# Kernel optimization log

Measured on AMD Instinct MI355X. Metric: run time of the kernel, lower is better.

Reference implementation:

```python
import jax, jax.numpy as jnp
import numpy as np

B, T, D, H = 512, 1024, 64, 64     # batch, time, input_size, hidden_size
R = 4                              # number of reward heads
MH = 32                            # MLP hidden size


def setup_inputs() -> dict:
    key = jax.random.key(0)
    ks = jax.random.split(key, 16)
    s = lambda k, shape, scale=1.0: jax.random.normal(k, shape, dtype=jnp.float32) * scale
    inp = {
        "x": s(ks[0], (B, T, D)),
        # learned initial states (nn.Parameter randn(1,1,H) -> store as (H,))
        "h_init": s(ks[1], (H,)),
        "c_init": s(ks[2], (H,)),
        # LSTM params, PyTorch layout: W_ih (4H, D), W_hh (4H, H), gate order i,f,g,o
        "W_ih": s(ks[3], (4 * H, D), 1.0 / np.sqrt(H)),
        "W_hh": s(ks[4], (4 * H, H), 1.0 / np.sqrt(H)),
        "b_ih": s(ks[5], (4 * H,), 1.0 / np.sqrt(H)),
        "b_hh": s(ks[6], (4 * H,), 1.0 / np.sqrt(H)),
        # R stacked MLP heads: Linear(H,MH) -> ReLU -> Linear(MH,MH) -> ReLU -> Linear(MH,1)
        "W1": s(ks[7], (R, MH, H), 1.0 / np.sqrt(H)),
        "b1": s(ks[8], (R, MH), 1.0 / np.sqrt(H)),
        "W2": s(ks[9], (R, MH, MH), 1.0 / np.sqrt(MH)),
        "b2": s(ks[10], (R, MH), 1.0 / np.sqrt(MH)),
        "W3": s(ks[11], (R, 1, MH), 1.0 / np.sqrt(MH)),
        "b3": s(ks[12], (R, 1), 1.0 / np.sqrt(MH)),
    }
    return inp


def _lstm(x, h0, c0, W_ih, W_hh, b_ih, b_hh):
    # x: (B, T, D). Returns y: (B, T, H).
    Hh = h0.shape[-1]
    b = b_ih + b_hh                      # (4H,)
    # precompute input projections for all steps: (T, B, 4H)
    xg = jnp.einsum('btd,gd->tbg', x, W_ih) + b

    def step(carry, xg_t):
        h, c = carry                     # (B, H) each
        gates = xg_t + h @ W_hh.T        # (B, 4H)
        i, f, g, o = jnp.split(gates, 4, axis=-1)
        c = jax.nn.sigmoid(f) * c + jax.nn.sigmoid(i) * jnp.tanh(g)
        h = jax.nn.sigmoid(o) * jnp.tanh(c)
        return (h, c), h

    Bb = x.shape[0]
    h0b = jnp.broadcast_to(h0, (Bb, Hh))
    c0b = jnp.broadcast_to(c0, (Bb, Hh))
    _, ys = jax.lax.scan(step, (h0b, c0b), xg)   # ys: (T, B, H)
    return jnp.transpose(ys, (1, 0, 2))


def _heads(y, W1, b1, W2, b2, W3, b3):
    # y: (B, T, H) -> (R, B, T); all R heads computed in one batched einsum chain
    h1 = jax.nn.relu(jnp.einsum('bth,rmh->rbtm', y, W1) + b1[:, None, None, :])
    h2 = jax.nn.relu(jnp.einsum('rbtm,rnm->rbtn', h1, W2) + b2[:, None, None, :])
    out = jnp.einsum('rbtn,ron->rbto', h2, W3) + b3[:, None, None, :]
    return out[..., 0]                   # squeeze last dim -> (R, B, T)


def reference(x, h_init, c_init, W_ih, W_hh, b_ih, b_hh, W1, b1, W2, b2, W3, b3):
    y = _lstm(x, h_init, c_init, W_ih, W_hh, b_ih, b_hh)
    outs = _heads(y, W1, b1, W2, b2, W3, b3)   # (R, B, T); row r == rewards[r] head
    return (y, outs)
```

## Files before the change

### kernel.cpp

```cpp
#include <hip/hip_runtime.h>

#define BB 512
#define TT 1024
#define DD 64
#define HH 64
#define BT (BB * TT)
#define Y_SIZE (BB * TT * HH)

typedef _Float16 half8 __attribute__((ext_vector_type(8)));
typedef _Float16 half4 __attribute__((ext_vector_type(4)));
typedef float f32x4 __attribute__((ext_vector_type(4)));

#define MFMA16(a, b, c) __builtin_amdgcn_mfma_f32_16x16x32_f16((a), (b), (c), 0, 0, 0)

__device__ __forceinline__ void wg_barrier_lds() {
    asm volatile("s_waitcnt lgkmcnt(0)" ::: "memory");
    __builtin_amdgcn_s_barrier();
    asm volatile("" ::: "memory");
}

__device__ __forceinline__ float sigm(float x) {
    return __builtin_amdgcn_rcpf(1.0f + __expf(-x));
}
__device__ __forceinline__ float tanh_(float x) {
    return 1.0f - 2.0f * __builtin_amdgcn_rcpf(1.0f + __expf(2.0f * x));
}

__device__ __forceinline__ half8 cvt8(f32x4 a, f32x4 b) {
    half8 h;
    h[0] = (_Float16)a[0]; h[1] = (_Float16)a[1];
    h[2] = (_Float16)a[2]; h[3] = (_Float16)a[3];
    h[4] = (_Float16)b[0]; h[5] = (_Float16)b[1];
    h[6] = (_Float16)b[2]; h[7] = (_Float16)b[3];
    return h;
}

__global__ __launch_bounds__(256) void lstm_kernel(
    const float* __restrict__ x, const float* __restrict__ h_init,
    const float* __restrict__ c_init, const float* __restrict__ W_ih,
    const float* __restrict__ W_hh, const float* __restrict__ b_ih,
    const float* __restrict__ b_hh, float* __restrict__ y)
{
    __shared__ alignas(16) _Float16 xch[2][16][2][72];
    __shared__ alignas(16) _Float16 hst[2][2][HH];
    __shared__ float xg[16][2][265];

    const int tid  = threadIdx.x;
    const int wave = tid >> 6;
    const int lane = tid & 63;
    const int col  = lane & 15;
    const int quad = lane >> 4;
    const int sel  = (lane >> 3) & 1;
    const int r_act = lane >> 5;
    const int j    = (wave << 4) + col;
    const bool writer = ((lane >> 4) & 1) == 0;

    const int b0 = blockIdx.x * 2;

    half8 bf[4][4];
    f32x4 biasv[4];
#pragma unroll
    for (int G = 0; G < 4; ++G) {
        const int n = (G << 6) + j;
        const float bs = b_ih[n] + b_hh[n];
        biasv[G][0] = bs; biasv[G][1] = bs; biasv[G][2] = bs; biasv[G][3] = bs;
#pragma unroll
        for (int c = 0; c < 4; ++c) {
            const float* src = (c < 2) ? (W_ih + n * DD + c * 32 + quad * 8)
                                       : (W_hh + n * HH + (c - 2) * 32 + quad * 8);
            f32x4 w0 = *(const f32x4*)src;
            f32x4 w1 = *(const f32x4*)(src + 4);
            bf[G][c] = cvt8(w0, w1);
        }
    }

    float c_state = c_init[j];

    if (tid < 128) {
        const int rr = tid >> 6, jj = tid & 63;
        hst[0][rr][jj] = (_Float16)h_init[jj];
    }
    {
        const int ss = tid >> 4, rr = (tid >> 3) & 1, j0 = (tid & 7) << 3;
        const float* src = x + ((b0 + rr) * TT + ss) * DD + j0;
        f32x4 g0 = *(const f32x4*)src;
        f32x4 g1 = *(const f32x4*)(src + 4);
        *(half8*)&xch[0][ss][rr][j0] = cvt8(g0, g1);
    }
    wg_barrier_lds();

    const int ss_pf = tid >> 4, rr_pf = (tid >> 3) & 1, j0_pf = (tid & 7) << 3;

    for (int ci = 0; ci < 64; ++ci) {
        const int buf = ci & 1;
        const bool pf = (ci + 1) < 64;
        f32x4 g0, g1;
        if (pf) {
            const float* src = x + ((b0 + rr_pf) * TT + ((ci + 1) << 4) + ss_pf) * DD + j0_pf;
            g0 = *(const f32x4*)src;
            g1 = *(const f32x4*)(src + 4);
        }

#pragma unroll
        for (int rr = 0; rr < 2; ++rr) {
            half8 ax0 = *(const half8*)&xch[buf][col][rr][quad * 8];
            half8 ax1 = *(const half8*)&xch[buf][col][rr][32 + quad * 8];
#pragma unroll
            for (int G = 0; G < 4; ++G) {
                f32x4 d = MFMA16(ax0, bf[G][0], biasv[G]);
                d = MFMA16(ax1, bf[G][1], d);
#pragma unroll
                for (int r = 0; r < 4; ++r)
                    xg[(quad << 2) + r][rr][(G << 6) + j] = d[r];
            }
        }

#pragma unroll
        for (int s = 0; s < 16; ++s) {
            const int t = (ci << 4) + s;
            const int p = s & 1;

            const float xg0 = xg[s][r_act][0 * 64 + j];
            const float xg1 = xg[s][r_act][1 * 64 + j];
            const float xg2 = xg[s][r_act][2 * 64 + j];
            const float xg3 = xg[s][r_act][3 * 64 + j];
            const _Float16* hrow = &hst[p][sel][0];
            half8 a2 = *(const half8*)(hrow + quad * 8);
            half8 a3 = *(const half8*)(hrow + 32 + quad * 8);

            f32x4 c0 = {xg0, xg0, xg0, xg0};
            f32x4 c1 = {xg1, xg1, xg1, xg1};
            f32x4 c2 = {xg2, xg2, xg2, xg2};
            f32x4 c3 = {xg3, xg3, xg3, xg3};
            f32x4 acc0 = MFMA16(a2, bf[0][2], c0);
            f32x4 acc1 = MFMA16(a2, bf[1][2], c1);
            f32x4 acc2 = MFMA16(a2, bf[2][2], c2);
            f32x4 acc3 = MFMA16(a2, bf[3][2], c3);
            acc0 = MFMA16(a3, bf[0][3], acc0); acc1 = MFMA16(a3, bf[1][3], acc1);
            acc2 = MFMA16(a3, bf[2][3], acc2); acc3 = MFMA16(a3, bf[3][3], acc3);

            const float si = sigm(acc0[0]);
            const float sf = sigm(acc1[0]);
            const float tg = tanh_(acc2[0]);
            const float so = sigm(acc3[0]);
            c_state = sf * c_state + si * tg;
            const float hv = so * tanh_(c_state);
            if (writer) {
                hst[p ^ 1][r_act][j] = (_Float16)hv;
                y[((b0 + r_act) * TT + t) * HH + j] = hv;
            }
            if (s == 14 && pf) {
                *(half8*)&xch[buf ^ 1][ss_pf][rr_pf][j0_pf] = cvt8(g0, g1);
            }
            wg_barrier_lds();
        }
    }
}

__global__ __launch_bounds__(256) void heads_kernel(
    const float* __restrict__ y,
    const float* __restrict__ W1, const float* __restrict__ b1,
    const float* __restrict__ W2, const float* __restrict__ b2,
    const float* __restrict__ W3, const float* __restrict__ b3,
    float* __restrict__ outs)
{
    __shared__ alignas(16) _Float16 h1w[4][2][16][144];
    __shared__ alignas(16) _Float16 h2w[4][2][16][144];

    const int tid  = threadIdx.x;
    const int wave = tid >> 6;
    const int lane = tid & 63;
    const int col  = lane & 15;
    const int quad = lane >> 4;

    half8 w1f[8][2]; float bias1[8];
#pragma unroll
    for (int nt = 0; nt < 8; ++nt) {
        const int n = nt * 16 + col;
        bias1[nt] = b1[n];
#pragma unroll
        for (int c = 0; c < 2; ++c) {
            const float* src = W1 + n * 64 + c * 32 + quad * 8;
            w1f[nt][c] = cvt8(*(const f32x4*)src, *(const f32x4*)(src + 4));
        }
    }
    half8 w2f[8]; float bias2[8];
#pragma unroll
    for (int nt = 0; nt < 8; ++nt) {
        const int n = nt * 16 + col;
        bias2[nt] = b2[n];
        const float* src = W2 + n * 32 + quad * 8;
        w2f[nt] = cvt8(*(const f32x4*)src, *(const f32x4*)(src + 4));
    }
    half8 b3f[4];
    {
        const float* src = W3 + (col < 4 ? col * 32 : 0) + quad * 8;
        half8 wv = cvt8(*(const f32x4*)src, *(const f32x4*)(src + 4));
        half8 hz;
#pragma unroll
        for (int i = 0; i < 8; ++i) hz[i] = (_Float16)0.0f;
#pragma unroll
        for (int kc = 0; kc < 4; ++kc)
            b3f[kc] = (col == kc) ? wv : hz;
    }
    const float b3v = (col < 4) ? b3[col] : 0.0f;

    const long wbase = (long)blockIdx.x * 256 + wave * 64;

    f32x4 ga0, ga1, ga2, ga3;
    {
        const float* src = y + (wbase + col) * 64 + quad * 8;
        ga0 = *(const f32x4*)src;       ga1 = *(const f32x4*)(src + 4);
        ga2 = *(const f32x4*)(src + 32); ga3 = *(const f32x4*)(src + 36);
    }

#pragma unroll
    for (int tb = 0; tb < 4; ++tb) {
        const int pb = tb & 1;
        half8 a0 = cvt8(ga0, ga1);
        half8 a1 = cvt8(ga2, ga3);
        if (tb < 3) {
            const float* src = y + (wbase + (tb + 1) * 16 + col) * 64 + quad * 8;
            ga0 = *(const f32x4*)src;       ga1 = *(const f32x4*)(src + 4);
            ga2 = *(const f32x4*)(src + 32); ga3 = *(const f32x4*)(src + 36);
        }

#pragma unroll
        for (int nt = 0; nt < 8; ++nt) {
            f32x4 acc = {bias1[nt], bias1[nt], bias1[nt], bias1[nt]};
            acc = MFMA16(a0, w1f[nt][0], acc);
            acc = MFMA16(a1, w1f[nt][1], acc);
#pragma unroll
            for (int r = 0; r < 4; ++r) {
                float v = acc[r] > 0.0f ? acc[r] : 0.0f;
                h1w[wave][pb][(quad << 2) + r][nt * 16 + col] = (_Float16)v;
            }
        }
        half8 ah[4];
#pragma unroll
        for (int hd = 0; hd < 4; ++hd)
            ah[hd] = *(const half8*)&h1w[wave][pb][col][hd * 32 + quad * 8];
#pragma unroll
        for (int nt = 0; nt < 8; ++nt) {
            f32x4 acc = {bias2[nt], bias2[nt], bias2[nt], bias2[nt]};
            acc = MFMA16(ah[nt >> 1], w2f[nt], acc);
#pragma unroll
            for (int r = 0; r < 4; ++r) {
                float v = acc[r] > 0.0f ? acc[r] : 0.0f;
                h2w[wave][pb][(quad << 2) + r][nt * 16 + col] = (_Float16)v;
            }
        }
        f32x4 d = {b3v, b3v, b3v, b3v};
#pragma unroll
        for (int kc = 0; kc < 4; ++kc) {
            half8 av = *(const half8*)&h2w[wave][pb][col][kc * 32 + quad * 8];
            d = MFMA16(av, b3f[kc], d);
        }
        if (col < 4)
            *(f32x4*)(outs + (long)col * BT + wbase + tb * 16 + quad * 4) = d;
    }
}

extern "C" void kernel_launch(void* const* d_in, const int* in_sizes, int n_in,
                              void* d_out, int out_size, void* d_ws, size_t ws_size,
                              hipStream_t stream) {
    (void)in_sizes; (void)n_in; (void)out_size; (void)d_ws; (void)ws_size;
    const float* x      = (const float*)d_in[0];
    const float* h_init = (const float*)d_in[1];
    const float* c_init = (const float*)d_in[2];
    const float* W_ih   = (const float*)d_in[3];
    const float* W_hh   = (const float*)d_in[4];
    const float* b_ih   = (const float*)d_in[5];
    const float* b_hh   = (const float*)d_in[6];
    const float* W1     = (const float*)d_in[7];
    const float* b1     = (const float*)d_in[8];
    const float* W2     = (const float*)d_in[9];
    const float* b2     = (const float*)d_in[10];
    const float* W3     = (const float*)d_in[11];
    const float* b3     = (const float*)d_in[12];
    float* y    = (float*)d_out;
    float* outs = y + Y_SIZE;

    lstm_kernel<<<dim3(256), dim3(256), 0, stream>>>(x, h_init, c_init, W_ih, W_hh,
                                                     b_ih, b_hh, y);
    heads_kernel<<<dim3(2048), dim3(256), 0, stream>>>(y, W1, b1, W2, b2, W3, b3, outs);
}
```

Before: 567.3 us.

## Fuse per-step input projection into recurrence, split gate activations, add fp16 y copy

```diff
diff --git a/kernel.cpp b/kernel.cpp
--- a/kernel.cpp
+++ b/kernel.cpp
@@ -24,6 +24,11 @@
 }
 __device__ __forceinline__ float tanh_(float x) {
     return 1.0f - 2.0f * __builtin_amdgcn_rcpf(1.0f + __expf(2.0f * x));
+}
+
+__device__ __forceinline__ float swz16(float x) {
+    return __int_as_float(
+        __builtin_amdgcn_ds_swizzle(__float_as_int(x), 0x401F));
 }
 
 __device__ __forceinline__ half8 cvt8(f32x4 a, f32x4 b) {
@@ -39,11 +44,11 @@
     const float* __restrict__ x, const float* __restrict__ h_init,
     const float* __restrict__ c_init, const float* __restrict__ W_ih,
     const float* __restrict__ W_hh, const float* __restrict__ b_ih,
-    const float* __restrict__ b_hh, float* __restrict__ y)
+    const float* __restrict__ b_hh, float* __restrict__ y,
+    _Float16* __restrict__ y16)
 {
-    __shared__ alignas(16) _Float16 xch[2][16][2][72];
+    __shared__ alignas(16) _Float16 xch[2][16][2][DD];
     __shared__ alignas(16) _Float16 hst[2][2][HH];
-    __shared__ float xg[16][2][265];
 
     const int tid  = threadIdx.x;
     const int wave = tid >> 6;
@@ -53,7 +58,8 @@
     const int sel  = (lane >> 3) & 1;
     const int r_act = lane >> 5;
     const int j    = (wave << 4) + col;
-    const bool writer = ((lane >> 4) & 1) == 0;
+    const int hi   = quad & 1;
+    const bool writer = (hi == 0);
 
     const int b0 = blockIdx.x * 2;
 
@@ -90,6 +96,17 @@
     wg_barrier_lds();
 
     const int ss_pf = tid >> 4, rr_pf = (tid >> 3) & 1, j0_pf = (tid & 7) << 3;
+
+    f32x4 xacc0, xacc1, xacc2, xacc3;
+    {
+        const _Float16* xrow = &xch[0][0][sel][0];
+        half8 a0 = *(const half8*)(xrow + quad * 8);
+        half8 a1 = *(const half8*)(xrow + 32 + quad * 8);
+        xacc0 = MFMA16(a0, bf[0][0], biasv[0]); xacc0 = MFMA16(a1, bf[0][1], xacc0);
+        xacc1 = MFMA16(a0, bf[1][0], biasv[1]); xacc1 = MFMA16(a1, bf[1][1], xacc1);
+        xacc2 = MFMA16(a0, bf[2][0], biasv[2]); xacc2 = MFMA16(a1, bf[2][1], xacc2);
+        xacc3 = MFMA16(a0, bf[3][0], biasv[3]); xacc3 = MFMA16(a1, bf[3][1], xacc3);
+    }
 
     for (int ci = 0; ci < 64; ++ci) {
         const int buf = ci & 1;
@@ -100,54 +117,48 @@
             g0 = *(const f32x4*)src;
             g1 = *(const f32x4*)(src + 4);
         }
-
-#pragma unroll
-        for (int rr = 0; rr < 2; ++rr) {
-            half8 ax0 = *(const half8*)&xch[buf][col][rr][quad * 8];
-            half8 ax1 = *(const half8*)&xch[buf][col][rr][32 + quad * 8];
-#pragma unroll
-            for (int G = 0; G < 4; ++G) {
-                f32x4 d = MFMA16(ax0, bf[G][0], biasv[G]);
-                d = MFMA16(ax1, bf[G][1], d);
-#pragma unroll
-                for (int r = 0; r < 4; ++r)
-                    xg[(quad << 2) + r][rr][(G << 6) + j] = d[r];
-            }
-        }
-
 #pragma unroll
         for (int s = 0; s < 16; ++s) {
             const int t = (ci << 4) + s;
             const int p = s & 1;
 
-            const float xg0 = xg[s][r_act][0 * 64 + j];
-            const float xg1 = xg[s][r_act][1 * 64 + j];
-            const float xg2 = xg[s][r_act][2 * 64 + j];
-            const float xg3 = xg[s][r_act][3 * 64 + j];
             const _Float16* hrow = &hst[p][sel][0];
             half8 a2 = *(const half8*)(hrow + quad * 8);
             half8 a3 = *(const half8*)(hrow + 32 + quad * 8);
-
-            f32x4 c0 = {xg0, xg0, xg0, xg0};
-            f32x4 c1 = {xg1, xg1, xg1, xg1};
-            f32x4 c2 = {xg2, xg2, xg2, xg2};
-            f32x4 c3 = {xg3, xg3, xg3, xg3};
-            f32x4 acc0 = MFMA16(a2, bf[0][2], c0);
-            f32x4 acc1 = MFMA16(a2, bf[1][2], c1);
-            f32x4 acc2 = MFMA16(a2, bf[2][2], c2);
-            f32x4 acc3 = MFMA16(a2, bf[3][2], c3);
+            f32x4 acc0 = MFMA16(a2, bf[0][2], xacc0);
+            f32x4 acc1 = MFMA16(a2, bf[1][2], xacc1);
+            f32x4 acc2 = MFMA16(a2, bf[2][2], xacc2);
+            f32x4 acc3 = MFMA16(a2, bf[3][2], xacc3);
             acc0 = MFMA16(a3, bf[0][3], acc0); acc1 = MFMA16(a3, bf[1][3], acc1);
             acc2 = MFMA16(a3, bf[2][3], acc2); acc3 = MFMA16(a3, bf[3][3], acc3);
 
-            const float si = sigm(acc0[0]);
-            const float sf = sigm(acc1[0]);
-            const float tg = tanh_(acc2[0]);
-            const float so = sigm(acc3[0]);
-            c_state = sf * c_state + si * tg;
-            const float hv = so * tanh_(c_state);
+            if (t < TT - 1) {
+                const _Float16* nx = (s < 15) ? &xch[buf][s + 1][sel][0]
+                                              : &xch[buf ^ 1][0][sel][0];
+                half8 a0 = *(const half8*)(nx + quad * 8);
+                half8 a1 = *(const half8*)(nx + 32 + quad * 8);
+                xacc0 = MFMA16(a0, bf[0][0], biasv[0]); xacc0 = MFMA16(a1, bf[0][1], xacc0);
+                xacc1 = MFMA16(a0, bf[1][0], biasv[1]); xacc1 = MFMA16(a1, bf[1][1], xacc1);
+                xacc2 = MFMA16(a0, bf[2][0], biasv[2]); xacc2 = MFMA16(a1, bf[2][1], xacc2);
+                xacc3 = MFMA16(a0, bf[3][0], biasv[3]); xacc3 = MFMA16(a1, bf[3][1], xacc3);
+            }
+
+            const float ua = hi ? (2.0f * acc2[0]) : (-acc0[0]);
+            const float ea = __expf(ua);
+            float av = __builtin_amdgcn_rcpf(1.0f + ea);
+            av = hi ? fmaf(-2.0f, av, 1.0f) : av;
+            const float vb = hi ? acc3[0] : acc1[0];
+            const float eb = __expf(-vb);
+            const float bv = __builtin_amdgcn_rcpf(1.0f + eb);
+            const float av_sw = swz16(av);
+            const float bv_sw = swz16(bv);
+            c_state = bv * c_state + av * av_sw;
+            const float hv = bv_sw * tanh_(c_state);
             if (writer) {
-                hst[p ^ 1][r_act][j] = (_Float16)hv;
+                const _Float16 hvh = (_Float16)hv;
+                hst[p ^ 1][r_act][j] = hvh;
                 y[((b0 + r_act) * TT + t) * HH + j] = hv;
+                if (y16) y16[((b0 + r_act) * TT + t) * HH + j] = hvh;
             }
             if (s == 14 && pf) {
                 *(half8*)&xch[buf ^ 1][ss_pf][rr_pf][j0_pf] = cvt8(g0, g1);
@@ -157,15 +168,112 @@
     }
 }
 
-__global__ __launch_bounds__(256) void heads_kernel(
+__global__ __launch_bounds__(256) void heads_kernel_f16(
+    const _Float16* __restrict__ y16,
+    const float* __restrict__ W1, const float* __restrict__ b1,
+    const float* __restrict__ W2, const float* __restrict__ b2,
+    const float* __restrict__ W3, const float* __restrict__ b3,
+    float* __restrict__ outs)
+{
+    __shared__ alignas(16) _Float16 h1w[4][16][144];
+    __shared__ alignas(16) _Float16 h2w[4][16][144];
+
+    const int tid  = threadIdx.x;
+    const int wave = tid >> 6;
+    const int lane = tid & 63;
+    const int col  = lane & 15;
+    const int quad = lane >> 4;
+
+    half8 w1f[8][2]; float bias1[8];
+#pragma unroll
+    for (int nt = 0; nt < 8; ++nt) {
+        const int n = nt * 16 + col;
+        bias1[nt] = b1[n];
+#pragma unroll
+        for (int c = 0; c < 2; ++c) {
+            const float* src = W1 + n * 64 + c * 32 + quad * 8;
+            w1f[nt][c] = cvt8(*(const f32x4*)src, *(const f32x4*)(src + 4));
+        }
+    }
+    half8 w2f[8]; float bias2[8];
+#pragma unroll
+    for (int nt = 0; nt < 8; ++nt) {
+        const int n = nt * 16 + col;
+        bias2[nt] = b2[n];
+        const float* src = W2 + n * 32 + quad * 8;
+        w2f[nt] = cvt8(*(const f32x4*)src, *(const f32x4*)(src + 4));
+    }
+    half8 b3f[4];
+    {
+        const float* src = W3 + (col < 4 ? col * 32 : 0) + quad * 8;
+        half8 wv = cvt8(*(const f32x4*)src, *(const f32x4*)(src + 4));
+        half8 hz;
+#pragma unroll
+        for (int i = 0; i < 8; ++i) hz[i] = (_Float16)0.0f;
+#pragma unroll
+        for (int kc = 0; kc < 4; ++kc)
+            b3f[kc] = (col == kc) ? wv : hz;
+    }
+    const float b3v = (col < 4) ? b3[col] : 0.0f;
+
+    const long wbase = (long)blockIdx.x * 256 + wave * 64;
+
+    half8 ga0 = *(const half8*)(y16 + (wbase + col) * 64 + quad * 8);
+    half8 ga1 = *(const half8*)(y16 + (wbase + col) * 64 + 32 + quad * 8);
+
+#pragma unroll
+    for (int tb = 0; tb < 4; ++tb) {
+        half8 a0 = ga0, a1 = ga1;
+        if (tb < 3) {
+            const _Float16* src = y16 + (wbase + (tb + 1) * 16 + col) * 64 + quad * 8;
+            ga0 = *(const half8*)src;
+            ga1 = *(const half8*)(src + 32);
+        }
+#pragma unroll
+        for (int nt = 0; nt < 8; ++nt) {
+            f32x4 acc = {bias1[nt], bias1[nt], bias1[nt], bias1[nt]};
+            acc = MFMA16(a0, w1f[nt][0], acc);
+            acc = MFMA16(a1, w1f[nt][1], acc);
+#pragma unroll
+            for (int r = 0; r < 4; ++r) {
+                float v = acc[r] > 0.0f ? acc[r] : 0.0f;
+                h1w[wave][(quad << 2) + r][nt * 16 + col] = (_Float16)v;
+            }
+        }
+        half8 ah[4];
+#pragma unroll
+        for (int hd = 0; hd < 4; ++hd)
+            ah[hd] = *(const half8*)&h1w[wave][col][hd * 32 + quad * 8];
+#pragma unroll
+        for (int nt = 0; nt < 8; ++nt) {
+            f32x4 acc = {bias2[nt], bias2[nt], bias2[nt], bias2[nt]};
+            acc = MFMA16(ah[nt >> 1], w2f[nt], acc);
+#pragma unroll
+            for (int r = 0; r < 4; ++r) {
+                float v = acc[r] > 0.0f ? acc[r] : 0.0f;
+                h2w[wave][(quad << 2) + r][nt * 16 + col] = (_Float16)v;
+            }
+        }
+        f32x4 d = {b3v, b3v, b3v, b3v};
+#pragma unroll
+        for (int kc = 0; kc < 4; ++kc) {
+            half8 av = *(const half8*)&h2w[wave][col][kc * 32 + quad * 8];
+            d = MFMA16(av, b3f[kc], d);
+        }
+        if (col < 4)
+            *(f32x4*)(outs + (long)col * BT + wbase + tb * 16 + quad * 4) = d;
+    }
+}
+
+__global__ __launch_bounds__(256) void heads_kernel_f32(
     const float* __restrict__ y,
     const float* __restrict__ W1, const float* __restrict__ b1,
     const float* __restrict__ W2, const float* __restrict__ b2,
     const float* __restrict__ W3, const float* __restrict__ b3,
     float* __restrict__ outs)
 {
-    __shared__ alignas(16) _Float16 h1w[4][2][16][144];
-    __shared__ alignas(16) _Float16 h2w[4][2][16][144];
+    __shared__ alignas(16) _Float16 h1w[4][16][144];
+    __shared__ alignas(16) _Float16 h2w[4][16][144];
 
     const int tid  = threadIdx.x;
     const int wave = tid >> 6;
@@ -210,21 +318,19 @@
     f32x4 ga0, ga1, ga2, ga3;
     {
         const float* src = y + (wbase + col) * 64 + quad * 8;
-        ga0 = *(const f32x4*)src;       ga1 = *(const f32x4*)(src + 4);
+        ga0 = *(const f32x4*)src;        ga1 = *(const f32x4*)(src + 4);
         ga2 = *(const f32x4*)(src + 32); ga3 = *(const f32x4*)(src + 36);
     }
 
 #pragma unroll
     for (int tb = 0; tb < 4; ++tb) {
-        const int pb = tb & 1;
         half8 a0 = cvt8(ga0, ga1);
         half8 a1 = cvt8(ga2, ga3);
         if (tb < 3) {
             const float* src = y + (wbase + (tb + 1) * 16 + col) * 64 + quad * 8;
-            ga0 = *(const f32x4*)src;       ga1 = *(const f32x4*)(src + 4);
+            ga0 = *(const f32x4*)src;        ga1 = *(const f32x4*)(src + 4);
             ga2 = *(const f32x4*)(src + 32); ga3 = *(const f32x4*)(src + 36);
         }
-
 #pragma unroll
         for (int nt = 0; nt < 8; ++nt) {
             f32x4 acc = {bias1[nt], bias1[nt], bias1[nt], bias1[nt]};
@@ -233,13 +339,13 @@
 #pragma unroll
             for (int r = 0; r < 4; ++r) {
                 float v = acc[r] > 0.0f ? acc[r] : 0.0f;
-                h1w[wave][pb][(quad << 2) + r][nt * 16 + col] = (_Float16)v;
+                h1w[wave][(quad << 2) + r][nt * 16 + col] = (_Float16)v;
             }
         }
         half8 ah[4];
 #pragma unroll
         for (int hd = 0; hd < 4; ++hd)
-            ah[hd] = *(const half8*)&h1w[wave][pb][col][hd * 32 + quad * 8];
+            ah[hd] = *(const half8*)&h1w[wave][col][hd * 32 + quad * 8];
 #pragma unroll
         for (int nt = 0; nt < 8; ++nt) {
             f32x4 acc = {bias2[nt], bias2[nt], bias2[nt], bias2[nt]};
@@ -247,13 +353,13 @@
 #pragma unroll
             for (int r = 0; r < 4; ++r) {
                 float v = acc[r] > 0.0f ? acc[r] : 0.0f;
-                h2w[wave][pb][(quad << 2) + r][nt * 16 + col] = (_Float16)v;
+                h2w[wave][(quad << 2) + r][nt * 16 + col] = (_Float16)v;
             }
         }
         f32x4 d = {b3v, b3v, b3v, b3v};
 #pragma unroll
         for (int kc = 0; kc < 4; ++kc) {
-            half8 av = *(const half8*)&h2w[wave][pb][col][kc * 32 + quad * 8];
+            half8 av = *(const half8*)&h2w[wave][col][kc * 32 + quad * 8];
             d = MFMA16(av, b3f[kc], d);
         }
         if (col < 4)
@@ -264,7 +370,7 @@
 extern "C" void kernel_launch(void* const* d_in, const int* in_sizes, int n_in,
                               void* d_out, int out_size, void* d_ws, size_t ws_size,
                               hipStream_t stream) {
-    (void)in_sizes; (void)n_in; (void)out_size; (void)d_ws; (void)ws_size;
+    (void)in_sizes; (void)n_in; (void)out_size;
     const float* x      = (const float*)d_in[0];
     const float* h_init = (const float*)d_in[1];
     const float* c_init = (const float*)d_in[2];
@@ -281,7 +387,15 @@
     float* y    = (float*)d_out;
     float* outs = y + Y_SIZE;
 
+    const bool use16 = (d_ws != nullptr) && (ws_size >= (size_t)Y_SIZE * 2);
+    _Float16* y16 = use16 ? (_Float16*)d_ws : nullptr;
+
     lstm_kernel<<<dim3(256), dim3(256), 0, stream>>>(x, h_init, c_init, W_ih, W_hh,
-                                                     b_ih, b_hh, y);
-    heads_kernel<<<dim3(2048), dim3(256), 0, stream>>>(y, W1, b1, W2, b2, W3, b3, outs);
-}
+                                                     b_ih, b_hh, y, y16);
+    if (use16)
+        heads_kernel_f16<<<dim3(2048), dim3(256), 0, stream>>>(y16, W1, b1, W2, b2,
+                                                               W3, b3, outs);
+    else
+        heads_kernel_f32<<<dim3(2048), dim3(256), 0, stream>>>(y, W1, b1, W2, b2,
+                                                               W3, b3, outs);
+}
```

Measured after the change: 584.9 us. +3.1%, slower.
